# Kernel tuning notes

Measured on AMD Instinct MI355X. Metric: run time of the kernel, lower is better.

Reference implementation:

```python
import jax, jax.numpy as jnp
import numpy as np

SORB = 64      # spin orbitals (sequence length)
NELE = 32      # electrons
H = 512        # num_hiddens
B = 4096       # batch
ALPHA = NELE // 2                      # = beta = 16 (spin-up / spin-down electrons)
MIN_I = min(SORB - 2 * ALPHA, 2 * ALPHA)  # = 32; symmetry mask active for i >= MIN_I
EPS = 1e-12


def setup_inputs() -> dict:
    key = jax.random.key(0)
    ks = jax.random.split(key, 10)
    s_in = 1.0 / np.sqrt(2.0)
    s_h = 1.0 / np.sqrt(H)
    return {
        "x": jax.random.randint(ks[0], (B, SORB), 0, 2, dtype=jnp.int32),  # occupancies {0,1}
        "W_ih0": jax.random.normal(ks[1], (3 * H, 2), jnp.float32) * s_in,   # GRU layer0 input weights (r,z,n)
        "W_hh0": jax.random.normal(ks[2], (3 * H, H), jnp.float32) * s_h,
        "W_ih1": jax.random.normal(ks[3], (3 * H, H), jnp.float32) * s_h,    # GRU layer1
        "W_hh1": jax.random.normal(ks[4], (3 * H, H), jnp.float32) * s_h,
        "W_amp": jax.random.normal(ks[5], (2, H), jnp.float32) * s_h,
        "b_amp": jax.random.normal(ks[6], (2,), jnp.float32) * 0.01,
        "W_phase": jax.random.normal(ks[7], (2, H), jnp.float32) * s_h,
        "b_phase": jax.random.normal(ks[8], (2,), jnp.float32) * 0.01,
    }


def _gru_cell(x_in, h, Wih, Whh):
    # PyTorch GRU (bias=False), gate order r, z, n
    gi = x_in @ Wih.T          # (B, 3H)
    gh = h @ Whh.T             # (B, 3H)
    r = jax.nn.sigmoid(gi[:, :H] + gh[:, :H])
    z = jax.nn.sigmoid(gi[:, H:2 * H] + gh[:, H:2 * H])
    n = jnp.tanh(gi[:, 2 * H:] + r * gh[:, 2 * H:])
    return (1.0 - z) * n + z * h


def reference(x, W_ih0, W_hh0, W_ih1, W_hh1, W_amp, b_amp, W_phase, b_phase):
    dt = W_ih0.dtype
    bits = x.astype(jnp.int32)           # (B, SORB) occupancies
    nb = bits.shape[0]

    def step(carry, inp):
        h0, h1, x0, amp, phase, nup, ndn = carry
        i, b_i = inp                      # site index, occupancy bits (B,)
        h0n = _gru_cell(x0, h0, W_ih0, W_hh0)
        h1n = _gru_cell(h0n, h1, W_ih1, W_hh1)
        y = h1n                           # (B, H)
        # amplitude: sqrt(softmax(linear))
        y_amp = jnp.sqrt(jax.nn.softmax(y @ W_amp.T + b_amp, axis=1))   # (B, 2)
        # phase: pi * softsign(linear)
        ph = y @ W_phase.T + b_phase
        y_ph = jnp.pi * ph / (1.0 + jnp.abs(ph))
        # particle-number symmetry mask (alpha == beta spin sectors)
        is_even = (i % 2) == 0            # even sites: spin-up, odd: spin-down
        cnt = jnp.where(is_even, nup, ndn)
        lower = (ALPHA - SORB // 2 + i // 2).astype(dt)
        occ_ok = (cnt < ALPHA).astype(dt)
        unocc_ok = (cnt > lower).astype(dt)
        mask = jnp.stack([unocc_ok, occ_ok], axis=1)
        masked = y_amp * mask
        masked = masked / jnp.sqrt(jnp.sum(masked * masked, axis=1, keepdims=True) + EPS)
        y_amp = jnp.where(i >= MIN_I, masked, y_amp)
        # accumulate conditional amplitude / phase at the sampled occupancy
        sel_a = jnp.take_along_axis(y_amp, b_i[:, None], axis=1)[:, 0]
        sel_p = jnp.take_along_axis(y_ph, b_i[:, None], axis=1)[:, 0]
        amp = amp * sel_a
        phase = phase + sel_p
        bf = b_i.astype(dt)
        nup = nup + jnp.where(is_even, bf, 0.0)
        ndn = ndn + jnp.where(is_even, 0.0, bf)
        x0n = jax.nn.one_hot(b_i, 2, dtype=dt)  # next-step GRU input
        return (h0n, h1n, x0n, amp, phase, nup, ndn), None

    init = (
        jnp.zeros((nb, H), dt), jnp.zeros((nb, H), dt), jnp.zeros((nb, 2), dt),
        jnp.ones((nb,), dt), jnp.zeros((nb,), dt), jnp.zeros((nb,), dt), jnp.zeros((nb,), dt),
    )
    xs = (jnp.arange(SORB), bits.T)       # scan over sites
    (_, _, _, amp, phase, _, _), _ = jax.lax.scan(step, init, xs)
    # complex wavefunction psi = amp * exp(1j*phase); returned as real pair (amp, phase)
    return jnp.stack([amp, phase], axis=-1)
```

## Files before the change

### kernel.cpp

```cpp
#include <hip/hip_runtime.h>
#include <hip/hip_bf16.h>

#define SORB  64
#define HID   512
#define BATCH 4096
#define N3H   1536
#define KD    512
#define BK    64
#define PI_F  3.14159265358979f

typedef _Float16 half8 __attribute__((ext_vector_type(8)));
typedef float    floatx4 __attribute__((ext_vector_type(4)));

__device__ __forceinline__ void gload16(const void* g, void* l) {
    __builtin_amdgcn_global_load_lds(
        (const __attribute__((address_space(1))) void*)g,
        (__attribute__((address_space(3))) void*)l, 16, 0, 0);
}

__device__ __forceinline__ float sigmoidf_(float x) { return 1.f / (1.f + __expf(-x)); }
__device__ __forceinline__ float tanhf_(float x) {
    x = fminf(fmaxf(x, -15.f), 15.f);
    const float e2 = __expf(2.f * x);
    return (e2 - 1.f) / (e2 + 1.f);
}

__global__ __launch_bounds__(256) void convw_kernel(
    const float* __restrict__ w0, const float* __restrict__ w1, const float* __restrict__ w2,
    _Float16* __restrict__ o0, _Float16* __restrict__ o1, _Float16* __restrict__ o2)
{
    const int i = blockIdx.x * 256 + threadIdx.x;
    if (i < N3H * KD) {
        o0[i] = (_Float16)w0[i];
        o1[i] = (_Float16)w1[i];
        o2[i] = (_Float16)w2[i];
    }
}

__global__ __launch_bounds__(256) void init_kernel(
    float* __restrict__ amp, float* __restrict__ phase,
    int* __restrict__ nup, int* __restrict__ ndn)
{
    const int i = blockIdx.x * 256 + threadIdx.x;
    if (i < BATCH) { amp[i] = 1.f; phase[i] = 0.f; nup[i] = 0; ndn[i] = 0; }
}

__device__ __forceinline__ void head_row(
    const _Float16* __restrict__ h1, int m,
    const float* __restrict__ Wamp, const float* __restrict__ bamp,
    const float* __restrict__ Wph,  const float* __restrict__ bph,
    const int* __restrict__ bits,
    float* __restrict__ amp, float* __restrict__ phase,
    int* __restrict__ nup, int* __restrict__ ndn,
    float* __restrict__ out, int step, int lane)
{
    const half8 hv = *(const half8*)(h1 + (size_t)m * HID + lane * 8);
    float d0 = 0.f, d1 = 0.f, d2 = 0.f, d3 = 0.f;
#pragma unroll
    for (int e = 0; e < 8; ++e) {
        const int j = lane * 8 + e;
        const float hn = (float)hv[e];
        d0 += hn * Wamp[j];       d1 += hn * Wamp[HID + j];
        d2 += hn * Wph[j];        d3 += hn * Wph[HID + j];
    }
#pragma unroll
    for (int off = 1; off < 64; off <<= 1) {
        d0 += __shfl_xor(d0, off); d1 += __shfl_xor(d1, off);
        d2 += __shfl_xor(d2, off); d3 += __shfl_xor(d3, off);
    }
    if (lane == 0) {
        const float a0 = d0 + bamp[0];
        const float a1 = d1 + bamp[1];
        const float mx = fmaxf(a0, a1);
        const float e0 = __expf(a0 - mx), e1 = __expf(a1 - mx);
        const float inv = 1.f / (e0 + e1);
        float ya0 = sqrtf(e0 * inv), ya1 = sqrtf(e1 * inv);
        const float p0 = d2 + bph[0];
        const float p1 = d3 + bph[1];
        const float yp0 = PI_F * p0 / (1.f + fabsf(p0));
        const float yp1 = PI_F * p1 / (1.f + fabsf(p1));
        const int even = ((step & 1) == 0);
        const int cnt = even ? nup[m] : ndn[m];
        if (step >= 32) {
            const int lower = (step >> 1) - 16;
            const float m0v = (cnt > lower) ? ya0 : 0.f;
            const float m1v = (cnt < 16) ? ya1 : 0.f;
            const float nrm = sqrtf(m0v * m0v + m1v * m1v + 1e-12f);
            ya0 = m0v / nrm; ya1 = m1v / nrm;
        }
        const int bi = bits[m * SORB + step];
        const float na = amp[m] * (bi ? ya1 : ya0);
        const float np = phase[m] + (bi ? yp1 : yp0);
        amp[m] = na; phase[m] = np;
        if (bi) { if (even) nup[m] = cnt + 1; else ndn[m] = cnt + 1; }
        if (step == SORB - 1) {
            out[m * 2 + 0] = na;
            out[m * 2 + 1] = np;
        }
    }
}

__global__ __launch_bounds__(256) void step1_kernel(
    const _Float16* __restrict__ h0h_c, const _Float16* __restrict__ h1h_c,
    const _Float16* __restrict__ wh0,   const _Float16* __restrict__ wh1,
    const float* __restrict__ Wih0, const int* __restrict__ bits,
    float* __restrict__ h0f, _Float16* __restrict__ h0h_n,
    _Float16* __restrict__ gB, int step,
    const float* __restrict__ Wamp, const float* __restrict__ bamp,
    const float* __restrict__ Wph,  const float* __restrict__ bph,
    float* __restrict__ amp, float* __restrict__ phase,
    int* __restrict__ nup, int* __restrict__ ndn, float* __restrict__ out)
{
    const int z = blockIdx.z;
    const _Float16* Aop = z ? h1h_c : h0h_c;
    const _Float16* Wop = z ? wh1 : wh0;
    const int j0 = blockIdx.x * 64;
    const int m0 = blockIdx.y * 64;

    __shared__ __align__(16) _Float16 As[64 * BK];
    __shared__ __align__(16) _Float16 Bs[192 * BK];

    const int tid  = threadIdx.x;
    const int lane = tid & 63;
    const int wid  = tid >> 6;
    const int wm   = wid >> 1, wj = wid & 1;
    const int ku   = lane >> 4;

    floatx4 acc[2][2][3];
    const floatx4 z4 = {0.f, 0.f, 0.f, 0.f};
#pragma unroll
    for (int a = 0; a < 2; ++a)
#pragma unroll
        for (int b = 0; b < 2; ++b)
#pragma unroll
            for (int g = 0; g < 3; ++g) acc[a][b][g] = z4;

    const _Float16* a_srcp[2];
#pragma unroll
    for (int k2 = 0; k2 < 2; ++k2) {
        const int p = tid + k2 * 256, row = p >> 3, c = (p & 7) ^ (row & 7);
        a_srcp[k2] = Aop + (size_t)(m0 + row) * KD + c * 8;
    }
    const _Float16* b_srcp[6];
#pragma unroll
    for (int k2 = 0; k2 < 6; ++k2) {
        const int p = tid + k2 * 256, row = p >> 3, c = (p & 7) ^ (row & 7);
        const int grow = (row >> 6) * HID + j0 + (row & 63);
        b_srcp[k2] = Wop + (size_t)grow * KD + c * 8;
    }
    _Float16* a_dst[2];
#pragma unroll
    for (int k2 = 0; k2 < 2; ++k2) a_dst[k2] = As + (size_t)(k2 * 256 + wid * 64) * 8;
    _Float16* b_dst[6];
#pragma unroll
    for (int k2 = 0; k2 < 6; ++k2) b_dst[k2] = Bs + (size_t)(k2 * 256 + wid * 64) * 8;

    int aoff[2][2], boff[2][3][2];
#pragma unroll
    for (int mf = 0; mf < 2; ++mf) {
        const int r = wm * 32 + mf * 16 + (lane & 15);
#pragma unroll
        for (int kk = 0; kk < 2; ++kk)
            aoff[mf][kk] = r * BK + (((kk * 4 + ku) ^ (r & 7)) * 8);
    }
#pragma unroll
    for (int jf = 0; jf < 2; ++jf)
#pragma unroll
        for (int g = 0; g < 3; ++g) {
            const int r = g * 64 + wj * 32 + jf * 16 + (lane & 15);
#pragma unroll
            for (int kk = 0; kk < 2; ++kk)
                boff[jf][g][kk] = r * BK + (((kk * 4 + ku) ^ (r & 7)) * 8);
        }

    for (int kt = 0; kt < 8; ++kt) {
        const int k0 = kt * BK;
#pragma unroll
        for (int k2 = 0; k2 < 2; ++k2) gload16(a_srcp[k2] + k0, a_dst[k2]);
#pragma unroll
        for (int k2 = 0; k2 < 6; ++k2) gload16(b_srcp[k2] + k0, b_dst[k2]);
        __syncthreads();
#pragma unroll
        for (int kk = 0; kk < 2; ++kk) {
            half8 af[2], bf[2][3];
#pragma unroll
            for (int mf = 0; mf < 2; ++mf) af[mf] = *(const half8*)(As + aoff[mf][kk]);
#pragma unroll
            for (int jf = 0; jf < 2; ++jf)
#pragma unroll
                for (int g = 0; g < 3; ++g) bf[jf][g] = *(const half8*)(Bs + boff[jf][g][kk]);
#pragma unroll
            for (int mf = 0; mf < 2; ++mf)
#pragma unroll
                for (int jf = 0; jf < 2; ++jf)
#pragma unroll
                    for (int g = 0; g < 3; ++g)
                        acc[mf][jf][g] = __builtin_amdgcn_mfma_f32_16x16x32_f16(
                            af[mf], bf[jf][g], acc[mf][jf][g], 0, 0, 0);
        }
        __syncthreads();
    }

    if (z == 0) {
#pragma unroll
        for (int mf = 0; mf < 2; ++mf)
#pragma unroll
            for (int jf = 0; jf < 2; ++jf) {
                const floatx4 gr = acc[mf][jf][0];
                const floatx4 gz = acc[mf][jf][1];
                const floatx4 gn = acc[mf][jf][2];
#pragma unroll
                for (int reg = 0; reg < 4; ++reg) {
                    const int m = m0 + wm * 32 + mf * 16 + (lane >> 4) * 4 + reg;
                    const int j = j0 + wj * 32 + jf * 16 + (lane & 15);
                    float gir = 0.f, giz = 0.f, gin = 0.f;
                    if (step > 0) {
                        const int tb = bits[m * SORB + step - 1];
                        gir = Wih0[j * 2 + tb];
                        giz = Wih0[(HID + j) * 2 + tb];
                        gin = Wih0[(2 * HID + j) * 2 + tb];
                    }
                    const float r  = sigmoidf_(gir + gr[reg]);
                    const float zz = sigmoidf_(giz + gz[reg]);
                    const float n  = tanhf_(gin + r * gn[reg]);
                    const size_t idx = (size_t)m * HID + j;
                    const float h  = h0f[idx];
                    const float hn = (1.f - zz) * n + zz * h;
                    h0f[idx]   = hn;
                    h0h_n[idx] = (_Float16)hn;
                }
            }
    } else {
#pragma unroll
        for (int mf = 0; mf < 2; ++mf)
#pragma unroll
            for (int jf = 0; jf < 2; ++jf)
#pragma unroll
                for (int g = 0; g < 3; ++g)
#pragma unroll
                    for (int reg = 0; reg < 4; ++reg) {
                        const int m = m0 + wm * 32 + mf * 16 + (lane >> 4) * 4 + reg;
                        const int j = j0 + wj * 32 + jf * 16 + (lane & 15);
                        gB[(size_t)m * N3H + g * HID + j] = (_Float16)acc[mf][jf][g][reg];
                    }
        if (step > 0) {
            const int t = blockIdx.y * 8 + blockIdx.x;
#pragma unroll
            for (int rr = 0; rr < 2; ++rr) {
                const int m = t * 8 + wid * 2 + rr;
                head_row(h1h_c, m, Wamp, bamp, Wph, bph, bits,
                         amp, phase, nup, ndn, out, step - 1, lane);
            }
        }
    }
}

__global__ __launch_bounds__(256) void step2_kernel(
    const _Float16* __restrict__ h0h_n, const _Float16* __restrict__ wi1,
    const _Float16* __restrict__ gB,
    float* __restrict__ h1f, _Float16* __restrict__ h1h_n)
{
    const int j0 = blockIdx.x * 64;
    const int m0 = blockIdx.y * 64;

    __shared__ __align__(16) _Float16 As[64 * BK];
    __shared__ __align__(16) _Float16 Bs[192 * BK];

    const int tid  = threadIdx.x;
    const int lane = tid & 63;
    const int wid  = tid >> 6;
    const int wm   = wid >> 1, wj = wid & 1;
    const int ku   = lane >> 4;

    floatx4 acc[2][2][3];
    const floatx4 z4 = {0.f, 0.f, 0.f, 0.f};
#pragma unroll
    for (int a = 0; a < 2; ++a)
#pragma unroll
        for (int b = 0; b < 2; ++b)
#pragma unroll
            for (int g = 0; g < 3; ++g) acc[a][b][g] = z4;

    const _Float16* a_srcp[2];
#pragma unroll
    for (int k2 = 0; k2 < 2; ++k2) {
        const int p = tid + k2 * 256, row = p >> 3, c = (p & 7) ^ (row & 7);
        a_srcp[k2] = h0h_n + (size_t)(m0 + row) * KD + c * 8;
    }
    const _Float16* b_srcp[6];
#pragma unroll
    for (int k2 = 0; k2 < 6; ++k2) {
        const int p = tid + k2 * 256, row = p >> 3, c = (p & 7) ^ (row & 7);
        const int grow = (row >> 6) * HID + j0 + (row & 63);
        b_srcp[k2] = wi1 + (size_t)grow * KD + c * 8;
    }
    _Float16* a_dst[2];
#pragma unroll
    for (int k2 = 0; k2 < 2; ++k2) a_dst[k2] = As + (size_t)(k2 * 256 + wid * 64) * 8;
    _Float16* b_dst[6];
#pragma unroll
    for (int k2 = 0; k2 < 6; ++k2) b_dst[k2] = Bs + (size_t)(k2 * 256 + wid * 64) * 8;

    int aoff[2][2], boff[2][3][2];
#pragma unroll
    for (int mf = 0; mf < 2; ++mf) {
        const int r = wm * 32 + mf * 16 + (lane & 15);
#pragma unroll
        for (int kk = 0; kk < 2; ++kk)
            aoff[mf][kk] = r * BK + (((kk * 4 + ku) ^ (r & 7)) * 8);
    }
#pragma unroll
    for (int jf = 0; jf < 2; ++jf)
#pragma unroll
        for (int g = 0; g < 3; ++g) {
            const int r = g * 64 + wj * 32 + jf * 16 + (lane & 15);
#pragma unroll
            for (int kk = 0; kk < 2; ++kk)
                boff[jf][g][kk] = r * BK + (((kk * 4 + ku) ^ (r & 7)) * 8);
        }

    for (int kt = 0; kt < 8; ++kt) {
        const int k0 = kt * BK;
#pragma unroll
        for (int k2 = 0; k2 < 2; ++k2) gload16(a_srcp[k2] + k0, a_dst[k2]);
#pragma unroll
        for (int k2 = 0; k2 < 6; ++k2) gload16(b_srcp[k2] + k0, b_dst[k2]);
        __syncthreads();
#pragma unroll
        for (int kk = 0; kk < 2; ++kk) {
            half8 af[2], bf[2][3];
#pragma unroll
            for (int mf = 0; mf < 2; ++mf) af[mf] = *(const half8*)(As + aoff[mf][kk]);
#pragma unroll
            for (int jf = 0; jf < 2; ++jf)
#pragma unroll
                for (int g = 0; g < 3; ++g) bf[jf][g] = *(const half8*)(Bs + boff[jf][g][kk]);
#pragma unroll
            for (int mf = 0; mf < 2; ++mf)
#pragma unroll
                for (int jf = 0; jf < 2; ++jf)
#pragma unroll
                    for (int g = 0; g < 3; ++g)
                        acc[mf][jf][g] = __builtin_amdgcn_mfma_f32_16x16x32_f16(
                            af[mf], bf[jf][g], acc[mf][jf][g], 0, 0, 0);
        }
        __syncthreads();
    }

#pragma unroll
    for (int mf = 0; mf < 2; ++mf)
#pragma unroll
        for (int jf = 0; jf < 2; ++jf) {
            const floatx4 gr = acc[mf][jf][0];
            const floatx4 gz = acc[mf][jf][1];
            const floatx4 gn = acc[mf][jf][2];
#pragma unroll
            for (int reg = 0; reg < 4; ++reg) {
                const int m = m0 + wm * 32 + mf * 16 + (lane >> 4) * 4 + reg;
                const int j = j0 + wj * 32 + jf * 16 + (lane & 15);
                const size_t gbase = (size_t)m * N3H;
                const float ghr = (float)gB[gbase + j];
                const float ghz = (float)gB[gbase + HID + j];
                const float ghn = (float)gB[gbase + 2 * HID + j];
                const float r  = sigmoidf_(gr[reg] + ghr);
                const float zz = sigmoidf_(gz[reg] + ghz);
                const float n  = tanhf_(gn[reg] + r * ghn);
                const size_t idx = (size_t)m * HID + j;
                const float h  = h1f[idx];
                const float hn = (1.f - zz) * n + zz * h;
                h1f[idx]   = hn;
                h1h_n[idx] = (_Float16)hn;
            }
        }
}

__global__ __launch_bounds__(256) void head_kernel(
    const _Float16* __restrict__ h1h_n,
    const float* __restrict__ Wamp, const float* __restrict__ bamp,
    const float* __restrict__ Wph,  const float* __restrict__ bph,
    const int* __restrict__ bits,
    float* __restrict__ amp, float* __restrict__ phase,
    int* __restrict__ nup, int* __restrict__ ndn,
    float* __restrict__ out, int step)
{
    const int lane = threadIdx.x & 63;
    const int m    = blockIdx.x * 4 + (threadIdx.x >> 6);
    head_row(h1h_n, m, Wamp, bamp, Wph, bph, bits, amp, phase, nup, ndn, out, step, lane);
}

extern "C" void kernel_launch(void* const* d_in, const int* in_sizes, int n_in,
                              void* d_out, int out_size, void* d_ws, size_t ws_size,
                              hipStream_t stream) {
    const int*   bits = (const int*)d_in[0];
    const float* Wih0 = (const float*)d_in[1];
    const float* Whh0 = (const float*)d_in[2];
    const float* Wih1 = (const float*)d_in[3];
    const float* Whh1 = (const float*)d_in[4];
    const float* Wamp = (const float*)d_in[5];
    const float* bamp = (const float*)d_in[6];
    const float* Wph  = (const float*)d_in[7];
    const float* bph  = (const float*)d_in[8];
    float* out = (float*)d_out;

    char* ws = (char*)d_ws;
    size_t off = 0;
    auto alloc = [&](size_t bytes) {
        void* p = ws + off;
        off = (off + bytes + 255) & ~(size_t)255;
        return p;
    };
    _Float16* wh0 = (_Float16*)alloc((size_t)N3H * KD * 2);
    _Float16* wi1 = (_Float16*)alloc((size_t)N3H * KD * 2);
    _Float16* wh1 = (_Float16*)alloc((size_t)N3H * KD * 2);
    float*    h0f = (float*)alloc((size_t)BATCH * HID * 4);
    float*    h1f = (float*)alloc((size_t)BATCH * HID * 4);
    _Float16* h0hA = (_Float16*)alloc((size_t)BATCH * HID * 2);
    _Float16* h0hB = (_Float16*)alloc((size_t)BATCH * HID * 2);
    _Float16* h1hA = (_Float16*)alloc((size_t)BATCH * HID * 2);
    _Float16* h1hB = (_Float16*)alloc((size_t)BATCH * HID * 2);
    _Float16* gB  = (_Float16*)alloc((size_t)BATCH * N3H * 2);
    float*    amp   = (float*)alloc((size_t)BATCH * 4);
    float*    phase = (float*)alloc((size_t)BATCH * 4);
    int*      nup   = (int*)alloc((size_t)BATCH * 4);
    int*      ndn   = (int*)alloc((size_t)BATCH * 4);

    _Float16* h0h[2] = {h0hA, h0hB};
    _Float16* h1h[2] = {h1hA, h1hB};

    hipMemsetAsync(h0f, 0, (size_t)BATCH * HID * 4, stream);
    hipMemsetAsync(h1f, 0, (size_t)BATCH * HID * 4, stream);
    hipMemsetAsync(h0hA, 0, (size_t)BATCH * HID * 2, stream);
    hipMemsetAsync(h1hA, 0, (size_t)BATCH * HID * 2, stream);
    convw_kernel<<<(N3H * KD + 255) / 256, 256, 0, stream>>>(Whh0, Wih1, Whh1, wh0, wi1, wh1);
    init_kernel<<<BATCH / 256, 256, 0, stream>>>(amp, phase, nup, ndn);

    for (int s = 0; s < SORB; ++s) {
        const int cur = s & 1, nxt = cur ^ 1;
        step1_kernel<<<dim3(8, 64, 2), 256, 0, stream>>>(
            h0h[cur], h1h[cur], wh0, wh1, Wih0, bits, h0f, h0h[nxt], gB, s,
            Wamp, bamp, Wph, bph, amp, phase, nup, ndn, out);
        step2_kernel<<<dim3(8, 64), 256, 0, stream>>>(
            h0h[nxt], wi1, gB, h1f, h1h[nxt]);
    }
    head_kernel<<<BATCH / 4, 256, 0, stream>>>(
        h1h[0], Wamp, bamp, Wph, bph, bits, amp, phase, nup, ndn, out, SORB - 1);
}
```

Baseline: 3.400 ms.

## Software-pipeline GRU layers and head across timesteps in one fused launch

```diff
diff --git a/kernel.cpp b/kernel.cpp
--- a/kernel.cpp
+++ b/kernel.cpp
@@ -100,25 +100,14 @@
     }
 }
 
-__global__ __launch_bounds__(256) void step1_kernel(
-    const _Float16* __restrict__ h0h_c, const _Float16* __restrict__ h1h_c,
-    const _Float16* __restrict__ wh0,   const _Float16* __restrict__ wh1,
+__device__ __forceinline__ void step1_body(
+    int tile, const _Float16* __restrict__ h0h_c, const _Float16* __restrict__ wh0,
     const float* __restrict__ Wih0, const int* __restrict__ bits,
-    float* __restrict__ h0f, _Float16* __restrict__ h0h_n,
-    _Float16* __restrict__ gB, int step,
-    const float* __restrict__ Wamp, const float* __restrict__ bamp,
-    const float* __restrict__ Wph,  const float* __restrict__ bph,
-    float* __restrict__ amp, float* __restrict__ phase,
-    int* __restrict__ nup, int* __restrict__ ndn, float* __restrict__ out)
-{
-    const int z = blockIdx.z;
-    const _Float16* Aop = z ? h1h_c : h0h_c;
-    const _Float16* Wop = z ? wh1 : wh0;
-    const int j0 = blockIdx.x * 64;
-    const int m0 = blockIdx.y * 64;
-
-    __shared__ __align__(16) _Float16 As[64 * BK];
-    __shared__ __align__(16) _Float16 Bs[192 * BK];
+    _Float16* __restrict__ h0h_n, int step,
+    _Float16* As, _Float16* Bs)
+{
+    const int j0 = (tile & 7) * 64;
+    const int m0 = (tile >> 3) * 64;
 
     const int tid  = threadIdx.x;
     const int lane = tid & 63;
@@ -139,14 +128,14 @@
 #pragma unroll
     for (int k2 = 0; k2 < 2; ++k2) {
         const int p = tid + k2 * 256, row = p >> 3, c = (p & 7) ^ (row & 7);
-        a_srcp[k2] = Aop + (size_t)(m0 + row) * KD + c * 8;
+        a_srcp[k2] = h0h_c + (size_t)(m0 + row) * KD + c * 8;
     }
     const _Float16* b_srcp[6];
 #pragma unroll
     for (int k2 = 0; k2 < 6; ++k2) {
         const int p = tid + k2 * 256, row = p >> 3, c = (p & 7) ^ (row & 7);
         const int grow = (row >> 6) * HID + j0 + (row & 63);
-        b_srcp[k2] = Wop + (size_t)grow * KD + c * 8;
+        b_srcp[k2] = wh0 + (size_t)grow * KD + c * 8;
     }
     _Float16* a_dst[2];
 #pragma unroll
@@ -201,70 +190,42 @@
         __syncthreads();
     }
 
-    if (z == 0) {
-#pragma unroll
-        for (int mf = 0; mf < 2; ++mf)
-#pragma unroll
-            for (int jf = 0; jf < 2; ++jf) {
-                const floatx4 gr = acc[mf][jf][0];
-                const floatx4 gz = acc[mf][jf][1];
-                const floatx4 gn = acc[mf][jf][2];
-#pragma unroll
-                for (int reg = 0; reg < 4; ++reg) {
-                    const int m = m0 + wm * 32 + mf * 16 + (lane >> 4) * 4 + reg;
-                    const int j = j0 + wj * 32 + jf * 16 + (lane & 15);
-                    float gir = 0.f, giz = 0.f, gin = 0.f;
-                    if (step > 0) {
-                        const int tb = bits[m * SORB + step - 1];
-                        gir = Wih0[j * 2 + tb];
-                        giz = Wih0[(HID + j) * 2 + tb];
-                        gin = Wih0[(2 * HID + j) * 2 + tb];
-                    }
-                    const float r  = sigmoidf_(gir + gr[reg]);
-                    const float zz = sigmoidf_(giz + gz[reg]);
-                    const float n  = tanhf_(gin + r * gn[reg]);
-                    const size_t idx = (size_t)m * HID + j;
-                    const float h  = h0f[idx];
-                    const float hn = (1.f - zz) * n + zz * h;
-                    h0f[idx]   = hn;
-                    h0h_n[idx] = (_Float16)hn;
+#pragma unroll
+    for (int mf = 0; mf < 2; ++mf)
+#pragma unroll
+        for (int jf = 0; jf < 2; ++jf) {
+            const floatx4 gr = acc[mf][jf][0];
+            const floatx4 gz = acc[mf][jf][1];
+            const floatx4 gn = acc[mf][jf][2];
+#pragma unroll
+            for (int reg = 0; reg < 4; ++reg) {
+                const int m = m0 + wm * 32 + mf * 16 + (lane >> 4) * 4 + reg;
+                const int j = j0 + wj * 32 + jf * 16 + (lane & 15);
+                float gir = 0.f, giz = 0.f, gin = 0.f;
+                if (step > 0) {
+                    const int tb = bits[m * SORB + step - 1];
+                    gir = Wih0[j * 2 + tb];
+                    giz = Wih0[(HID + j) * 2 + tb];
+                    gin = Wih0[(2 * HID + j) * 2 + tb];
                 }
+                const float r  = sigmoidf_(gir + gr[reg]);
+                const float zz = sigmoidf_(giz + gz[reg]);
+                const float n  = tanhf_(gin + r * gn[reg]);
+                const size_t idx = (size_t)m * HID + j;
+                const float h  = (float)h0h_c[idx];
+                h0h_n[idx] = (_Float16)((1.f - zz) * n + zz * h);
             }
-    } else {
-#pragma unroll
-        for (int mf = 0; mf < 2; ++mf)
-#pragma unroll
-            for (int jf = 0; jf < 2; ++jf)
-#pragma unroll
-                for (int g = 0; g < 3; ++g)
-#pragma unroll
-                    for (int reg = 0; reg < 4; ++reg) {
-                        const int m = m0 + wm * 32 + mf * 16 + (lane >> 4) * 4 + reg;
-                        const int j = j0 + wj * 32 + jf * 16 + (lane & 15);
-                        gB[(size_t)m * N3H + g * HID + j] = (_Float16)acc[mf][jf][g][reg];
-                    }
-        if (step > 0) {
-            const int t = blockIdx.y * 8 + blockIdx.x;
-#pragma unroll
-            for (int rr = 0; rr < 2; ++rr) {
-                const int m = t * 8 + wid * 2 + rr;
-                head_row(h1h_c, m, Wamp, bamp, Wph, bph, bits,
-                         amp, phase, nup, ndn, out, step - 1, lane);
-            }
-        }
-    }
-}
-
-__global__ __launch_bounds__(256) void step2_kernel(
-    const _Float16* __restrict__ h0h_n, const _Float16* __restrict__ wi1,
-    const _Float16* __restrict__ gB,
-    float* __restrict__ h1f, _Float16* __restrict__ h1h_n)
-{
-    const int j0 = blockIdx.x * 64;
-    const int m0 = blockIdx.y * 64;
-
-    __shared__ __align__(16) _Float16 As[64 * BK];
-    __shared__ __align__(16) _Float16 Bs[192 * BK];
+        }
+}
+
+__device__ __forceinline__ void step2_body(
+    int tile, const _Float16* __restrict__ h0h_n, const _Float16* __restrict__ h1h_c,
+    const _Float16* __restrict__ wi1, const _Float16* __restrict__ wh1,
+    _Float16* __restrict__ h1h_n,
+    _Float16* As, _Float16* Bs)
+{
+    const int j0 = (tile & 7) * 64;
+    const int m0 = (tile >> 3) * 64;
 
     const int tid  = threadIdx.x;
     const int lane = tid & 63;
@@ -273,27 +234,17 @@
     const int ku   = lane >> 4;
 
     floatx4 acc[2][2][3];
+    floatx4 accn[2][2];
     const floatx4 z4 = {0.f, 0.f, 0.f, 0.f};
 #pragma unroll
     for (int a = 0; a < 2; ++a)
 #pragma unroll
-        for (int b = 0; b < 2; ++b)
+        for (int b = 0; b < 2; ++b) {
 #pragma unroll
             for (int g = 0; g < 3; ++g) acc[a][b][g] = z4;
-
-    const _Float16* a_srcp[2];
-#pragma unroll
-    for (int k2 = 0; k2 < 2; ++k2) {
-        const int p = tid + k2 * 256, row = p >> 3, c = (p & 7) ^ (row & 7);
-        a_srcp[k2] = h0h_n + (size_t)(m0 + row) * KD + c * 8;
-    }
-    const _Float16* b_srcp[6];
-#pragma unroll
-    for (int k2 = 0; k2 < 6; ++k2) {
-        const int p = tid + k2 * 256, row = p >> 3, c = (p & 7) ^ (row & 7);
-        const int grow = (row >> 6) * HID + j0 + (row & 63);
-        b_srcp[k2] = wi1 + (size_t)grow * KD + c * 8;
-    }
+            accn[a][b] = z4;
+        }
+
     _Float16* a_dst[2];
 #pragma unroll
     for (int k2 = 0; k2 < 2; ++k2) a_dst[k2] = As + (size_t)(k2 * 256 + wid * 64) * 8;
@@ -319,59 +270,113 @@
                 boff[jf][g][kk] = r * BK + (((kk * 4 + ku) ^ (r & 7)) * 8);
         }
 
-    for (int kt = 0; kt < 8; ++kt) {
-        const int k0 = kt * BK;
-#pragma unroll
-        for (int k2 = 0; k2 < 2; ++k2) gload16(a_srcp[k2] + k0, a_dst[k2]);
-#pragma unroll
-        for (int k2 = 0; k2 < 6; ++k2) gload16(b_srcp[k2] + k0, b_dst[k2]);
-        __syncthreads();
-#pragma unroll
-        for (int kk = 0; kk < 2; ++kk) {
-            half8 af[2], bf[2][3];
-#pragma unroll
-            for (int mf = 0; mf < 2; ++mf) af[mf] = *(const half8*)(As + aoff[mf][kk]);
-#pragma unroll
-            for (int jf = 0; jf < 2; ++jf)
-#pragma unroll
-                for (int g = 0; g < 3; ++g) bf[jf][g] = *(const half8*)(Bs + boff[jf][g][kk]);
-#pragma unroll
-            for (int mf = 0; mf < 2; ++mf)
+#pragma unroll 1
+    for (int half = 0; half < 2; ++half) {
+        const _Float16* Aop = half ? h1h_c : h0h_n;
+        const _Float16* Wop = half ? wh1  : wi1;
+        const _Float16* a_srcp[2];
+#pragma unroll
+        for (int k2 = 0; k2 < 2; ++k2) {
+            const int p = tid + k2 * 256, row = p >> 3, c = (p & 7) ^ (row & 7);
+            a_srcp[k2] = Aop + (size_t)(m0 + row) * KD + c * 8;
+        }
+        const _Float16* b_srcp[6];
+#pragma unroll
+        for (int k2 = 0; k2 < 6; ++k2) {
+            const int p = tid + k2 * 256, row = p >> 3, c = (p & 7) ^ (row & 7);
+            const int grow = (row >> 6) * HID + j0 + (row & 63);
+            b_srcp[k2] = Wop + (size_t)grow * KD + c * 8;
+        }
+
+        for (int kt = 0; kt < 8; ++kt) {
+            const int k0 = kt * BK;
+#pragma unroll
+            for (int k2 = 0; k2 < 2; ++k2) gload16(a_srcp[k2] + k0, a_dst[k2]);
+#pragma unroll
+            for (int k2 = 0; k2 < 6; ++k2) gload16(b_srcp[k2] + k0, b_dst[k2]);
+            __syncthreads();
+#pragma unroll
+            for (int kk = 0; kk < 2; ++kk) {
+                half8 af[2], bf[2][3];
+#pragma unroll
+                for (int mf = 0; mf < 2; ++mf) af[mf] = *(const half8*)(As + aoff[mf][kk]);
 #pragma unroll
                 for (int jf = 0; jf < 2; ++jf)
 #pragma unroll
-                    for (int g = 0; g < 3; ++g)
-                        acc[mf][jf][g] = __builtin_amdgcn_mfma_f32_16x16x32_f16(
-                            af[mf], bf[jf][g], acc[mf][jf][g], 0, 0, 0);
-        }
-        __syncthreads();
+                    for (int g = 0; g < 3; ++g) bf[jf][g] = *(const half8*)(Bs + boff[jf][g][kk]);
+#pragma unroll
+                for (int mf = 0; mf < 2; ++mf)
+#pragma unroll
+                    for (int jf = 0; jf < 2; ++jf) {
+                        acc[mf][jf][0] = __builtin_amdgcn_mfma_f32_16x16x32_f16(
+                            af[mf], bf[jf][0], acc[mf][jf][0], 0, 0, 0);
+                        acc[mf][jf][1] = __builtin_amdgcn_mfma_f32_16x16x32_f16(
+                            af[mf], bf[jf][1], acc[mf][jf][1], 0, 0, 0);
+                        if (half == 0)
+                            acc[mf][jf][2] = __builtin_amdgcn_mfma_f32_16x16x32_f16(
+                                af[mf], bf[jf][2], acc[mf][jf][2], 0, 0, 0);
+                        else
+                            accn[mf][jf] = __builtin_amdgcn_mfma_f32_16x16x32_f16(
+                                af[mf], bf[jf][2], accn[mf][jf], 0, 0, 0);
+                    }
+            }
+            __syncthreads();
+        }
     }
 
 #pragma unroll
     for (int mf = 0; mf < 2; ++mf)
 #pragma unroll
         for (int jf = 0; jf < 2; ++jf) {
-            const floatx4 gr = acc[mf][jf][0];
-            const floatx4 gz = acc[mf][jf][1];
-            const floatx4 gn = acc[mf][jf][2];
+            const floatx4 grz = acc[mf][jf][0];
+            const floatx4 gzz = acc[mf][jf][1];
+            const floatx4 gin = acc[mf][jf][2];
+            const floatx4 ghn = accn[mf][jf];
 #pragma unroll
             for (int reg = 0; reg < 4; ++reg) {
                 const int m = m0 + wm * 32 + mf * 16 + (lane >> 4) * 4 + reg;
                 const int j = j0 + wj * 32 + jf * 16 + (lane & 15);
-                const size_t gbase = (size_t)m * N3H;
-                const float ghr = (float)gB[gbase + j];
-                const float ghz = (float)gB[gbase + HID + j];
-                const float ghn = (float)gB[gbase + 2 * HID + j];
-                const float r  = sigmoidf_(gr[reg] + ghr);
-                const float zz = sigmoidf_(gz[reg] + ghz);
-                const float n  = tanhf_(gn[reg] + r * ghn);
+                const float r  = sigmoidf_(grz[reg]);
+                const float zz = sigmoidf_(gzz[reg]);
+                const float n  = tanhf_(gin[reg] + r * ghn[reg]);
                 const size_t idx = (size_t)m * HID + j;
-                const float h  = h1f[idx];
-                const float hn = (1.f - zz) * n + zz * h;
-                h1f[idx]   = hn;
-                h1h_n[idx] = (_Float16)hn;
+                const float h  = (float)h1h_c[idx];
+                h1h_n[idx] = (_Float16)((1.f - zz) * n + zz * h);
             }
         }
+}
+
+__global__ __launch_bounds__(256) void fat_kernel(
+    const _Float16* __restrict__ h0h_c, _Float16* __restrict__ h0h_n,
+    const _Float16* __restrict__ h1h_p, _Float16* __restrict__ h1h_w,
+    const _Float16* __restrict__ wh0, const _Float16* __restrict__ wi1,
+    const _Float16* __restrict__ wh1,
+    const float* __restrict__ Wih0, const int* __restrict__ bits,
+    const float* __restrict__ Wamp, const float* __restrict__ bamp,
+    const float* __restrict__ Wph,  const float* __restrict__ bph,
+    float* __restrict__ amp, float* __restrict__ phase,
+    int* __restrict__ nup, int* __restrict__ ndn, float* __restrict__ out, int s)
+{
+    __shared__ __align__(16) _Float16 As[64 * BK];
+    __shared__ __align__(16) _Float16 Bs[192 * BK];
+
+    const int bid = blockIdx.x;
+    if (bid < 512) {
+        if (s >= SORB) return;
+        step1_body(bid, h0h_c, wh0, Wih0, bits, h0h_n, s, As, Bs);
+    } else if (bid < 1024) {
+        if (s < 1) return;
+        step2_body(bid - 512, h0h_c, h1h_p, wi1, wh1, h1h_w, As, Bs);
+    } else {
+        if (s < 2) return;
+        const int lane = threadIdx.x & 63;
+        const int wid  = threadIdx.x >> 6;
+        const int base = (bid - 1024) * 32 + wid * 8;
+#pragma unroll
+        for (int rr = 0; rr < 8; ++rr)
+            head_row(h1h_p, base + rr, Wamp, bamp, Wph, bph, bits,
+                     amp, phase, nup, ndn, out, s - 2, lane);
+    }
 }
 
 __global__ __launch_bounds__(256) void head_kernel(
@@ -412,13 +417,10 @@
     _Float16* wh0 = (_Float16*)alloc((size_t)N3H * KD * 2);
     _Float16* wi1 = (_Float16*)alloc((size_t)N3H * KD * 2);
     _Float16* wh1 = (_Float16*)alloc((size_t)N3H * KD * 2);
-    float*    h0f = (float*)alloc((size_t)BATCH * HID * 4);
-    float*    h1f = (float*)alloc((size_t)BATCH * HID * 4);
     _Float16* h0hA = (_Float16*)alloc((size_t)BATCH * HID * 2);
     _Float16* h0hB = (_Float16*)alloc((size_t)BATCH * HID * 2);
     _Float16* h1hA = (_Float16*)alloc((size_t)BATCH * HID * 2);
     _Float16* h1hB = (_Float16*)alloc((size_t)BATCH * HID * 2);
-    _Float16* gB  = (_Float16*)alloc((size_t)BATCH * N3H * 2);
     float*    amp   = (float*)alloc((size_t)BATCH * 4);
     float*    phase = (float*)alloc((size_t)BATCH * 4);
     int*      nup   = (int*)alloc((size_t)BATCH * 4);
@@ -427,20 +429,18 @@
     _Float16* h0h[2] = {h0hA, h0hB};
     _Float16* h1h[2] = {h1hA, h1hB};
 
-    hipMemsetAsync(h0f, 0, (size_t)BATCH * HID * 4, stream);
-    hipMemsetAsync(h1f, 0, (size_t)BATCH * HID * 4, stream);
     hipMemsetAsync(h0hA, 0, (size_t)BATCH * HID * 2, stream);
     hipMemsetAsync(h1hA, 0, (size_t)BATCH * HID * 2, stream);
     convw_kernel<<<(N3H * KD + 255) / 256, 256, 0, stream>>>(Whh0, Wih1, Whh1, wh0, wi1, wh1);
     init_kernel<<<BATCH / 256, 256, 0, stream>>>(amp, phase, nup, ndn);
 
-    for (int s = 0; s < SORB; ++s) {
-        const int cur = s & 1, nxt = cur ^ 1;
-        step1_kernel<<<dim3(8, 64, 2), 256, 0, stream>>>(
-            h0h[cur], h1h[cur], wh0, wh1, Wih0, bits, h0f, h0h[nxt], gB, s,
-            Wamp, bamp, Wph, bph, amp, phase, nup, ndn, out);
-        step2_kernel<<<dim3(8, 64), 256, 0, stream>>>(
-            h0h[nxt], wi1, gB, h1f, h1h[nxt]);
+    for (int s = 0; s <= SORB; ++s) {
+        const int cur = s & 1;
+        fat_kernel<<<1152, 256, 0, stream>>>(
+            h0h[cur], h0h[cur ^ 1],
+            h1h[cur ^ 1], h1h[cur],
+            wh0, wi1, wh1, Wih0, bits,
+            Wamp, bamp, Wph, bph, amp, phase, nup, ndn, out, s);
     }
     head_kernel<<<BATCH / 4, 256, 0, stream>>>(
         h1h[0], Wamp, bamp, Wph, bph, bits, amp, phase, nup, ndn, out, SORB - 1);
```

Result: faster. 3.089 ms (-9.1%).

## Drop fp32 hidden-state copies and move head rows into dedicated extra blocks

Applied to the files above, without the earlier changes.

```diff
diff --git a/kernel.cpp b/kernel.cpp
--- a/kernel.cpp
+++ b/kernel.cpp
@@ -104,27 +104,40 @@
     const _Float16* __restrict__ h0h_c, const _Float16* __restrict__ h1h_c,
     const _Float16* __restrict__ wh0,   const _Float16* __restrict__ wh1,
     const float* __restrict__ Wih0, const int* __restrict__ bits,
-    float* __restrict__ h0f, _Float16* __restrict__ h0h_n,
-    _Float16* __restrict__ gB, int step,
+    _Float16* __restrict__ h0h_n, _Float16* __restrict__ gB, int step,
     const float* __restrict__ Wamp, const float* __restrict__ bamp,
     const float* __restrict__ Wph,  const float* __restrict__ bph,
     float* __restrict__ amp, float* __restrict__ phase,
     int* __restrict__ nup, int* __restrict__ ndn, float* __restrict__ out)
 {
-    const int z = blockIdx.z;
-    const _Float16* Aop = z ? h1h_c : h0h_c;
-    const _Float16* Wop = z ? wh1 : wh0;
-    const int j0 = blockIdx.x * 64;
-    const int m0 = blockIdx.y * 64;
-
-    __shared__ __align__(16) _Float16 As[64 * BK];
-    __shared__ __align__(16) _Float16 Bs[192 * BK];
-
+    const int bid  = blockIdx.x;
     const int tid  = threadIdx.x;
     const int lane = tid & 63;
     const int wid  = tid >> 6;
-    const int wm   = wid >> 1, wj = wid & 1;
-    const int ku   = lane >> 4;
+
+    if (bid >= 1024) {
+        if (step > 0) {
+            const int base = (bid - 1024) * 32 + wid * 8;
+#pragma unroll
+            for (int rr = 0; rr < 8; ++rr)
+                head_row(h1h_c, base + rr, Wamp, bamp, Wph, bph, bits,
+                         amp, phase, nup, ndn, out, step - 1, lane);
+        }
+        return;
+    }
+
+    const int z  = bid >> 9;
+    const int t  = bid & 511;
+    const int j0 = (t & 7) * 64;
+    const int m0 = (t >> 3) * 64;
+    const _Float16* Aop = z ? h1h_c : h0h_c;
+    const _Float16* Wop = z ? wh1 : wh0;
+
+    __shared__ __align__(16) _Float16 As[64 * BK];
+    __shared__ __align__(16) _Float16 Bs[192 * BK];
+
+    const int wm = wid >> 1, wj = wid & 1;
+    const int ku = lane >> 4;
 
     floatx4 acc[2][2][3];
     const floatx4 z4 = {0.f, 0.f, 0.f, 0.f};
@@ -224,10 +237,8 @@
                     const float zz = sigmoidf_(giz + gz[reg]);
                     const float n  = tanhf_(gin + r * gn[reg]);
                     const size_t idx = (size_t)m * HID + j;
-                    const float h  = h0f[idx];
-                    const float hn = (1.f - zz) * n + zz * h;
-                    h0f[idx]   = hn;
-                    h0h_n[idx] = (_Float16)hn;
+                    const float h  = (float)h0h_c[idx];
+                    h0h_n[idx] = (_Float16)((1.f - zz) * n + zz * h);
                 }
             }
     } else {
@@ -243,22 +254,13 @@
                         const int j = j0 + wj * 32 + jf * 16 + (lane & 15);
                         gB[(size_t)m * N3H + g * HID + j] = (_Float16)acc[mf][jf][g][reg];
                     }
-        if (step > 0) {
-            const int t = blockIdx.y * 8 + blockIdx.x;
-#pragma unroll
-            for (int rr = 0; rr < 2; ++rr) {
-                const int m = t * 8 + wid * 2 + rr;
-                head_row(h1h_c, m, Wamp, bamp, Wph, bph, bits,
-                         amp, phase, nup, ndn, out, step - 1, lane);
-            }
-        }
     }
 }
 
 __global__ __launch_bounds__(256) void step2_kernel(
-    const _Float16* __restrict__ h0h_n, const _Float16* __restrict__ wi1,
-    const _Float16* __restrict__ gB,
-    float* __restrict__ h1f, _Float16* __restrict__ h1h_n)
+    const _Float16* __restrict__ h0h_n, const _Float16* __restrict__ h1h_c,
+    const _Float16* __restrict__ wi1,   const _Float16* __restrict__ gB,
+    _Float16* __restrict__ h1h_n)
 {
     const int j0 = blockIdx.x * 64;
     const int m0 = blockIdx.y * 64;
@@ -366,10 +368,8 @@
                 const float zz = sigmoidf_(gz[reg] + ghz);
                 const float n  = tanhf_(gn[reg] + r * ghn);
                 const size_t idx = (size_t)m * HID + j;
-                const float h  = h1f[idx];
-                const float hn = (1.f - zz) * n + zz * h;
-                h1f[idx]   = hn;
-                h1h_n[idx] = (_Float16)hn;
+                const float h  = (float)h1h_c[idx];
+                h1h_n[idx] = (_Float16)((1.f - zz) * n + zz * h);
             }
         }
 }
@@ -412,13 +412,11 @@
     _Float16* wh0 = (_Float16*)alloc((size_t)N3H * KD * 2);
     _Float16* wi1 = (_Float16*)alloc((size_t)N3H * KD * 2);
     _Float16* wh1 = (_Float16*)alloc((size_t)N3H * KD * 2);
-    float*    h0f = (float*)alloc((size_t)BATCH * HID * 4);
-    float*    h1f = (float*)alloc((size_t)BATCH * HID * 4);
     _Float16* h0hA = (_Float16*)alloc((size_t)BATCH * HID * 2);
     _Float16* h0hB = (_Float16*)alloc((size_t)BATCH * HID * 2);
     _Float16* h1hA = (_Float16*)alloc((size_t)BATCH * HID * 2);
     _Float16* h1hB = (_Float16*)alloc((size_t)BATCH * HID * 2);
-    _Float16* gB  = (_Float16*)alloc((size_t)BATCH * N3H * 2);
+    _Float16* gB   = (_Float16*)alloc((size_t)BATCH * N3H * 2);
     float*    amp   = (float*)alloc((size_t)BATCH * 4);
     float*    phase = (float*)alloc((size_t)BATCH * 4);
     int*      nup   = (int*)alloc((size_t)BATCH * 4);
@@ -427,8 +425,6 @@
     _Float16* h0h[2] = {h0hA, h0hB};
     _Float16* h1h[2] = {h1hA, h1hB};
 
-    hipMemsetAsync(h0f, 0, (size_t)BATCH * HID * 4, stream);
-    hipMemsetAsync(h1f, 0, (size_t)BATCH * HID * 4, stream);
     hipMemsetAsync(h0hA, 0, (size_t)BATCH * HID * 2, stream);
     hipMemsetAsync(h1hA, 0, (size_t)BATCH * HID * 2, stream);
     convw_kernel<<<(N3H * KD + 255) / 256, 256, 0, stream>>>(Whh0, Wih1, Whh1, wh0, wi1, wh1);
@@ -436,11 +432,11 @@
 
     for (int s = 0; s < SORB; ++s) {
         const int cur = s & 1, nxt = cur ^ 1;
-        step1_kernel<<<dim3(8, 64, 2), 256, 0, stream>>>(
-            h0h[cur], h1h[cur], wh0, wh1, Wih0, bits, h0f, h0h[nxt], gB, s,
+        step1_kernel<<<1152, 256, 0, stream>>>(
+            h0h[cur], h1h[cur], wh0, wh1, Wih0, bits, h0h[nxt], gB, s,
             Wamp, bamp, Wph, bph, amp, phase, nup, ndn, out);
         step2_kernel<<<dim3(8, 64), 256, 0, stream>>>(
-            h0h[nxt], wi1, gB, h1f, h1h[nxt]);
+            h0h[nxt], h1h[cur], wi1, gB, h1h[nxt]);
     }
     head_kernel<<<BATCH / 4, 256, 0, stream>>>(
         h1h[0], Wamp, bamp, Wph, bph, bits, amp, phase, nup, ndn, out, SORB - 1);
```

After: 2.764 ms. 18.7% less time.
